# Performance work log

Hardware: AMD Instinct MI355X
Metric: run time of the kernel (lower is better)

The kernel has to match this reference:

```python
import jax, jax.numpy as jnp
import numpy as np

N, E, D_IN, D_OUT = 50000, 800000, 128, 64


def setup_inputs() -> dict:
    key = jax.random.key(0)
    ks = jax.random.split(key, 8)
    s = 1.0 / np.sqrt(D_IN)
    return {
        "x": jax.random.normal(ks[0], (N, D_IN), jnp.float32),
        "edge_index": jax.random.randint(ks[1], (2, E), 0, N),
        "edge_weight": jax.random.uniform(ks[2], (E,), jnp.float32),
        "init_w": jax.random.normal(ks[3], (D_IN, D_IN), jnp.float32) * s,
        "gru_w_ih": jax.random.normal(ks[4], (3 * D_IN, D_IN), jnp.float32) * s,
        "gru_w_hh": jax.random.normal(ks[5], (3 * D_IN, D_IN), jnp.float32) * s,
        "gru_b_ih": jnp.zeros((3 * D_IN,), jnp.float32),
        "gru_b_hh": jnp.zeros((3 * D_IN,), jnp.float32),
        "lin_w": jax.random.normal(ks[6], (D_OUT, D_IN), jnp.float32) * s,
        "lin_b": jnp.zeros((D_OUT,), jnp.float32),
    }


def _gru_step(x, h, w_ih, w_hh, b_ih, b_hh):
    # torch GRU gate order: r, z, n
    gi = x @ w_ih.T + b_ih
    gh = h @ w_hh.T + b_hh
    i_r, i_z, i_n = jnp.split(gi, 3, axis=-1)
    h_r, h_z, h_n = jnp.split(gh, 3, axis=-1)
    r = jax.nn.sigmoid(i_r + h_r)
    z = jax.nn.sigmoid(i_z + h_z)
    n = jnp.tanh(i_n + r * h_n)
    return (1.0 - z) * n + z * h


def reference(x, edge_index, edge_weight, init_w, gru_w_ih, gru_w_hh, gru_b_ih, gru_b_hh, lin_w, lin_b):
    n_nodes = x.shape[0]
    # EvolveGCNO: evolve W via one GRU step, W is both input and hidden (rows = GRU batch)
    W = _gru_step(init_w, init_w, gru_w_ih, gru_w_hh, gru_b_ih, gru_b_hh)  # [D_IN, D_IN]

    # gcn_norm with self-loops (fill value 1.0)
    loop = jnp.arange(n_nodes)
    row = jnp.concatenate([edge_index[0], loop])  # source j
    col = jnp.concatenate([edge_index[1], loop])  # target i
    w = jnp.concatenate([edge_weight, jnp.ones((n_nodes,), x.dtype)])
    deg = jax.ops.segment_sum(w, col, num_segments=n_nodes)
    dis = jnp.where(deg > 0, jax.lax.rsqrt(jnp.maximum(deg, 1e-12)), 0.0)
    norm = dis[row] * w * dis[col]  # [E+N]

    xw = x @ W  # [N, D_IN]
    h = jax.ops.segment_sum(norm[:, None] * xw[row], col, num_segments=n_nodes)
    h = jax.nn.relu(h)
    return h @ lin_w.T + lin_b  # [N, D_OUT]
```

## Files before the change

kernel.cpp:

```cpp
#include <hip/hip_runtime.h>
#include <hip/hip_fp16.h>
#include <math.h>

#define NN 50000
#define NE 800000
#define D  128
#define D3 384
#define DO 64

__global__ __launch_bounds__(256) void gru_matmul_kernel(
    const float* __restrict__ init_w, const float* __restrict__ w_ih,
    const float* __restrict__ w_hh, const float* __restrict__ b_ih,
    const float* __restrict__ b_hh, float* __restrict__ gi, float* __restrict__ gh) {
  int idx = blockIdx.x * 256 + threadIdx.x;
  if (idx >= D * D3) return;
  int b = idx / D3;
  int g = idx % D3;
  const float* xr = init_w + b * D;
  const float* wi = w_ih + g * D;
  const float* wh = w_hh + g * D;
  float ai = 0.f, ah = 0.f;
#pragma unroll 8
  for (int k = 0; k < D; ++k) {
    float xv = xr[k];
    ai += xv * wi[k];
    ah += xv * wh[k];
  }
  gi[idx] = ai + b_ih[g];
  gh[idx] = ah + b_hh[g];
}

__global__ __launch_bounds__(256) void gru_combine_kernel(
    const float* __restrict__ gi, const float* __restrict__ gh,
    const float* __restrict__ init_w, float* __restrict__ W) {
  int idx = blockIdx.x * 256 + threadIdx.x;
  if (idx >= D * D) return;
  int b = idx / D;
  int j = idx % D;
  float ir = gi[b * D3 + j],          hr = gh[b * D3 + j];
  float iz = gi[b * D3 + D + j],      hz = gh[b * D3 + D + j];
  float in_ = gi[b * D3 + 2 * D + j], hn = gh[b * D3 + 2 * D + j];
  float r = 1.f / (1.f + expf(-(ir + hr)));
  float z = 1.f / (1.f + expf(-(iz + hz)));
  float n = tanhf(in_ + r * hn);
  W[idx] = (1.f - z) * n + z * init_w[idx];
}

__global__ __launch_bounds__(256) void init_kernel(unsigned long long* __restrict__ packed,
                                                   int* __restrict__ total) {
  int i = blockIdx.x * 256 + threadIdx.x;
  if (i < NN) packed[i] = (1ULL << 32);
  if (i == 0) *total = 0;
}

__global__ __launch_bounds__(256) void count_deg_kernel(const int* __restrict__ col,
                                                        const float* __restrict__ ew,
                                                        unsigned long long* __restrict__ packed,
                                                        int* __restrict__ rank) {
  int e = blockIdx.x * 256 + threadIdx.x;
  if (e < NE) {
    int c = col[e];
    unsigned long long add =
        (1ULL << 40) | (unsigned long long)(ew[e] * 4294967296.0f);
    unsigned long long old = atomicAdd(&packed[c], add);
    rank[e] = (int)(old >> 40);
  }
}

__global__ __launch_bounds__(256) void dis_scan_kernel(
    const unsigned long long* __restrict__ packed, float* __restrict__ dis,
    int* __restrict__ cnt, int* __restrict__ start, int* __restrict__ total) {
  int i = blockIdx.x * 256 + threadIdx.x;
  int lane = threadIdx.x & 63;
  int c = 0;
  float d = 1.0f;
  if (i < NN) {
    unsigned long long p = packed[i];
    c = (int)(p >> 40);
    d = (float)(p & ((1ULL << 40) - 1)) * 0x1p-32f;
  }
  int pre = c;
#pragma unroll
  for (int off = 1; off < 64; off <<= 1) {
    int t = __shfl_up(pre, off, 64);
    if (lane >= off) pre += t;
  }
  int excl = pre - c;
  int wtot = __shfl(pre, 63, 64);
  int base = 0;
  if (lane == 63) base = atomicAdd(total, wtot);
  base = __shfl(base, 63, 64);
  if (i < NN) {
    start[i] = base + excl;
    cnt[i] = c;
    dis[i] = rsqrtf(fmaxf(d, 1e-12f));
  }
}

__global__ __launch_bounds__(256) void bucket_kernel(
    const int* __restrict__ row, const int* __restrict__ col,
    const float* __restrict__ ew, const int* __restrict__ rank,
    const float* __restrict__ dis, const int* __restrict__ start,
    int2* __restrict__ elist) {
  int e = blockIdx.x * 256 + threadIdx.x;
  if (e >= NE) return;
  int j = row[e];
  int c = col[e];
  float nrm = dis[j] * ew[e] * dis[c];
  int slot = start[c] + rank[e];
  elist[slot] = make_int2(j, __float_as_int(nrm));
}

struct alignas(16) h2x4 { __half2 a, b, c, d; };

__global__ __launch_bounds__(256) void xw_kernel(const float* __restrict__ x,
                                                 const float* __restrict__ W,
                                                 __half* __restrict__ xwh) {
  __shared__ float Wl[D * D];
  for (int i = threadIdx.x; i < D * D; i += 256) Wl[i] = W[i];
  __syncthreads();
  const int t = threadIdx.x;
  const int rr = t >> 4;
  const int c0 = (t & 15) * 8;
  const int ROWS_PER_TILE = 64;
  for (int base = blockIdx.x * ROWS_PER_TILE; base < NN; base += gridDim.x * ROWS_PER_TILE) {
    float acc[4][8];
#pragma unroll
    for (int q = 0; q < 4; ++q)
#pragma unroll
      for (int j = 0; j < 8; ++j) acc[q][j] = 0.f;
    int r0 = base + rr;
#pragma unroll 4
    for (int k = 0; k < D; ++k) {
      float xv[4];
#pragma unroll
      for (int q = 0; q < 4; ++q) {
        int r = r0 + q * 16;
        xv[q] = (r < NN) ? x[(long)r * D + k] : 0.f;
      }
#pragma unroll
      for (int j = 0; j < 8; ++j) {
        float wv = Wl[k * D + c0 + j];
#pragma unroll
        for (int q = 0; q < 4; ++q) acc[q][j] += xv[q] * wv;
      }
    }
#pragma unroll
    for (int q = 0; q < 4; ++q) {
      int r = r0 + q * 16;
      if (r < NN) {
        h2x4 pk;
        pk.a = __floats2half2_rn(acc[q][0], acc[q][1]);
        pk.b = __floats2half2_rn(acc[q][2], acc[q][3]);
        pk.c = __floats2half2_rn(acc[q][4], acc[q][5]);
        pk.d = __floats2half2_rn(acc[q][6], acc[q][7]);
        *(h2x4*)(xwh + (long)r * D + c0) = pk;
      }
    }
  }
}

__global__ __launch_bounds__(256) void gather_out_kernel(
    const int* __restrict__ start, const int* __restrict__ cnt,
    const int2* __restrict__ elist, const float* __restrict__ dis,
    const __half* __restrict__ xwh, const float* __restrict__ lin_w,
    const float* __restrict__ lin_b, float* __restrict__ out) {
  __shared__ __half2 LTh[(D / 2) * DO];
  __shared__ float hb[4][D];
  for (int idx = threadIdx.x; idx < (D / 2) * DO; idx += 256) {
    int kk = idx >> 6, o = idx & 63;
    LTh[idx] = __floats2half2_rn(lin_w[o * D + 2 * kk], lin_w[o * D + 2 * kk + 1]);
  }
  __syncthreads();
  const int wv = threadIdx.x >> 6;
  const int lane = threadIdx.x & 63;
  const float bias = lin_b[lane];
  const __half2* __restrict__ xw2 = (const __half2*)xwh;
  int gw = blockIdx.x * 4 + wv;
  int nw = gridDim.x * 4;
  for (int i = gw; i < NN; i += nw) {
    float ds = dis[i];
    float sn = ds * ds;
    float2 sv = __half22float2(xw2[(long)i * 64 + lane]);
    float a0 = sn * sv.x;
    float a1 = sn * sv.y;
    int s = start[i];
    int se = s + cnt[i];
    for (; s + 4 <= se; s += 4) {
      int2 e0 = elist[s], e1 = elist[s + 1], e2 = elist[s + 2], e3 = elist[s + 3];
      __half2 v0 = xw2[(long)e0.x * 64 + lane];
      __half2 v1 = xw2[(long)e1.x * 64 + lane];
      __half2 v2 = xw2[(long)e2.x * 64 + lane];
      __half2 v3 = xw2[(long)e3.x * 64 + lane];
      float n0 = __int_as_float(e0.y), n1 = __int_as_float(e1.y);
      float n2 = __int_as_float(e2.y), n3 = __int_as_float(e3.y);
      float2 f0 = __half22float2(v0), f1 = __half22float2(v1);
      float2 f2 = __half22float2(v2), f3 = __half22float2(v3);
      a0 += n0 * f0.x + n1 * f1.x + n2 * f2.x + n3 * f3.x;
      a1 += n0 * f0.y + n1 * f1.y + n2 * f2.y + n3 * f3.y;
    }
    for (; s < se; ++s) {
      int2 e0 = elist[s];
      float2 f0 = __half22float2(xw2[(long)e0.x * 64 + lane]);
      float n0 = __int_as_float(e0.y);
      a0 += n0 * f0.x;
      a1 += n0 * f0.y;
    }
    *(float2*)&hb[wv][2 * lane] = make_float2(fmaxf(a0, 0.f), fmaxf(a1, 0.f));
    asm volatile("s_waitcnt lgkmcnt(0)" ::: "memory");
    float acc = bias;
#pragma unroll
    for (int kk = 0; kk < D / 2; ++kk) {
      float2 hv = *(const float2*)&hb[wv][2 * kk];
      float2 wf = __half22float2(LTh[kk * DO + lane]);
      acc += hv.x * wf.x + hv.y * wf.y;
    }
    asm volatile("s_waitcnt lgkmcnt(0)" ::: "memory");
    out[(long)i * DO + lane] = acc;
  }
}

extern "C" void kernel_launch(void* const* d_in, const int* in_sizes, int n_in,
                              void* d_out, int out_size, void* d_ws, size_t ws_size,
                              hipStream_t stream) {
  const float* x      = (const float*)d_in[0];
  const int*   eidx   = (const int*)d_in[1];
  const float* ew     = (const float*)d_in[2];
  const float* init_w = (const float*)d_in[3];
  const float* w_ih   = (const float*)d_in[4];
  const float* w_hh   = (const float*)d_in[5];
  const float* b_ih   = (const float*)d_in[6];
  const float* b_hh   = (const float*)d_in[7];
  const float* lin_w  = (const float*)d_in[8];
  const float* lin_b  = (const float*)d_in[9];
  float* out = (float*)d_out;
  const int* row = eidx;
  const int* col = eidx + NE;

  float* ws    = (float*)d_ws;
  float* W     = ws;
  float* gi    = W + 16384;
  float* gh    = gi + 49152;
  unsigned long long* packed = (unsigned long long*)(gh + 49152);
  float* dis   = (float*)(packed + 50048);
  int*   cnt   = (int*)(dis + 50048);
  int*   strt  = cnt + 50048;
  int*   total = strt + 50048;
  int*   rank  = total + 64;
  int2*  elist = (int2*)(rank + NE);
  __half* xwh  = (__half*)(elist + NE);

  gru_matmul_kernel<<<192, 256, 0, stream>>>(init_w, w_ih, w_hh, b_ih, b_hh, gi, gh);
  gru_combine_kernel<<<64, 256, 0, stream>>>(gi, gh, init_w, W);
  init_kernel<<<(NN + 255) / 256, 256, 0, stream>>>(packed, total);
  count_deg_kernel<<<(NE + 255) / 256, 256, 0, stream>>>(col, ew, packed, rank);
  xw_kernel<<<512, 256, 0, stream>>>(x, W, xwh);
  dis_scan_kernel<<<(NN + 255) / 256, 256, 0, stream>>>(packed, dis, cnt, strt, total);
  bucket_kernel<<<(NE + 255) / 256, 256, 0, stream>>>(row, col, ew, rank, dis, strt,
                                                      elist);
  gather_out_kernel<<<2048, 256, 0, stream>>>(strt, cnt, elist, dis, xwh,
                                              lin_w, lin_b, out);
}
```

Measured before the change: 192.9 us.

## Fuse GRU setup, align edge buckets, split gather from output projection

The two GRU kernels and the init kernel are merged into one setup kernel, so gi/gh no longer round-trip through global memory. Bucket starts are padded to even counts so the gather can read edge pairs with 16-byte vector loads. Streaming loads and stores are marked nontemporal. The gather no longer does the per-node linear layer through LDS: it writes ReLU'd h in fp16, and a separate kernel applies lin_w using fdot2 with the weights held in registers. The cost is an extra fp16 intermediate of N×128 written and read back, plus one more kernel launch.

```diff
diff --git a/kernel.cpp b/kernel.cpp
--- a/kernel.cpp
+++ b/kernel.cpp
@@ -8,49 +8,57 @@
 #define D3 384
 #define DO 64
 
-__global__ __launch_bounds__(256) void gru_matmul_kernel(
+typedef _Float16 f16x2 __attribute__((ext_vector_type(2)));
+
+__device__ __forceinline__ float dot2acc(unsigned int h2bits, f16x2 w, float acc) {
+#if __has_builtin(__builtin_amdgcn_fdot2)
+  return __builtin_amdgcn_fdot2(__builtin_bit_cast(f16x2, h2bits), w, acc, false);
+#else
+  __half2 h = __builtin_bit_cast(__half2, h2bits);
+  float2 hf = __half22float2(h);
+  return acc + hf.x * (float)w[0] + hf.y * (float)w[1];
+#endif
+}
+
+__global__ __launch_bounds__(256) void setup_kernel(
     const float* __restrict__ init_w, const float* __restrict__ w_ih,
     const float* __restrict__ w_hh, const float* __restrict__ b_ih,
-    const float* __restrict__ b_hh, float* __restrict__ gi, float* __restrict__ gh) {
+    const float* __restrict__ b_hh, float* __restrict__ W,
+    unsigned long long* __restrict__ packed, int* __restrict__ total) {
+  if (blockIdx.x >= 64) {
+    int i = (blockIdx.x - 64) * 256 + threadIdx.x;
+    if (i < NN) packed[i] = (1ULL << 32);
+    if (i == 0) *total = 0;
+    return;
+  }
   int idx = blockIdx.x * 256 + threadIdx.x;
-  if (idx >= D * D3) return;
-  int b = idx / D3;
-  int g = idx % D3;
+  int b = idx >> 7;
+  int j = idx & 127;
   const float* xr = init_w + b * D;
-  const float* wi = w_ih + g * D;
-  const float* wh = w_hh + g * D;
-  float ai = 0.f, ah = 0.f;
-#pragma unroll 8
+  const float* wr_i = w_ih + j * D;
+  const float* wz_i = w_ih + (D + j) * D;
+  const float* wn_i = w_ih + (2 * D + j) * D;
+  const float* wr_h = w_hh + j * D;
+  const float* wz_h = w_hh + (D + j) * D;
+  const float* wn_h = w_hh + (2 * D + j) * D;
+  float ir = 0.f, iz = 0.f, in_ = 0.f, hr = 0.f, hz = 0.f, hn = 0.f;
+#pragma unroll 4
   for (int k = 0; k < D; ++k) {
     float xv = xr[k];
-    ai += xv * wi[k];
-    ah += xv * wh[k];
-  }
-  gi[idx] = ai + b_ih[g];
-  gh[idx] = ah + b_hh[g];
-}
-
-__global__ __launch_bounds__(256) void gru_combine_kernel(
-    const float* __restrict__ gi, const float* __restrict__ gh,
-    const float* __restrict__ init_w, float* __restrict__ W) {
-  int idx = blockIdx.x * 256 + threadIdx.x;
-  if (idx >= D * D) return;
-  int b = idx / D;
-  int j = idx % D;
-  float ir = gi[b * D3 + j],          hr = gh[b * D3 + j];
-  float iz = gi[b * D3 + D + j],      hz = gh[b * D3 + D + j];
-  float in_ = gi[b * D3 + 2 * D + j], hn = gh[b * D3 + 2 * D + j];
+    ir += xv * wr_i[k];
+    iz += xv * wz_i[k];
+    in_ += xv * wn_i[k];
+    hr += xv * wr_h[k];
+    hz += xv * wz_h[k];
+    hn += xv * wn_h[k];
+  }
+  ir += b_ih[j];       hr += b_hh[j];
+  iz += b_ih[D + j];   hz += b_hh[D + j];
+  in_ += b_ih[2 * D + j]; hn += b_hh[2 * D + j];
   float r = 1.f / (1.f + expf(-(ir + hr)));
   float z = 1.f / (1.f + expf(-(iz + hz)));
   float n = tanhf(in_ + r * hn);
   W[idx] = (1.f - z) * n + z * init_w[idx];
-}
-
-__global__ __launch_bounds__(256) void init_kernel(unsigned long long* __restrict__ packed,
-                                                   int* __restrict__ total) {
-  int i = blockIdx.x * 256 + threadIdx.x;
-  if (i < NN) packed[i] = (1ULL << 32);
-  if (i == 0) *total = 0;
 }
 
 __global__ __launch_bounds__(256) void count_deg_kernel(const int* __restrict__ col,
@@ -59,11 +67,11 @@
                                                         int* __restrict__ rank) {
   int e = blockIdx.x * 256 + threadIdx.x;
   if (e < NE) {
-    int c = col[e];
-    unsigned long long add =
-        (1ULL << 40) | (unsigned long long)(ew[e] * 4294967296.0f);
+    int c = __builtin_nontemporal_load(&col[e]);
+    float w = __builtin_nontemporal_load(&ew[e]);
+    unsigned long long add = (1ULL << 40) | (unsigned long long)(w * 4294967296.0f);
     unsigned long long old = atomicAdd(&packed[c], add);
-    rank[e] = (int)(old >> 40);
+    __builtin_nontemporal_store((int)(old >> 40), &rank[e]);
   }
 }
 
@@ -79,13 +87,14 @@
     c = (int)(p >> 40);
     d = (float)(p & ((1ULL << 40) - 1)) * 0x1p-32f;
   }
-  int pre = c;
+  int cp = (c + 1) & ~1;
+  int pre = cp;
 #pragma unroll
   for (int off = 1; off < 64; off <<= 1) {
     int t = __shfl_up(pre, off, 64);
     if (lane >= off) pre += t;
   }
-  int excl = pre - c;
+  int excl = pre - cp;
   int wtot = __shfl(pre, 63, 64);
   int base = 0;
   if (lane == 63) base = atomicAdd(total, wtot);
@@ -104,10 +113,12 @@
     int2* __restrict__ elist) {
   int e = blockIdx.x * 256 + threadIdx.x;
   if (e >= NE) return;
-  int j = row[e];
-  int c = col[e];
-  float nrm = dis[j] * ew[e] * dis[c];
-  int slot = start[c] + rank[e];
+  int j = __builtin_nontemporal_load(&row[e]);
+  int c = __builtin_nontemporal_load(&col[e]);
+  float w = __builtin_nontemporal_load(&ew[e]);
+  int rk = __builtin_nontemporal_load(&rank[e]);
+  float nrm = dis[j] * w * dis[c];
+  int slot = start[c] + rk;
   elist[slot] = make_int2(j, __float_as_int(nrm));
 }
 
@@ -160,22 +171,14 @@
   }
 }
 
-__global__ __launch_bounds__(256) void gather_out_kernel(
+__global__ __launch_bounds__(256) void gather_h_kernel(
     const int* __restrict__ start, const int* __restrict__ cnt,
     const int2* __restrict__ elist, const float* __restrict__ dis,
-    const __half* __restrict__ xwh, const float* __restrict__ lin_w,
-    const float* __restrict__ lin_b, float* __restrict__ out) {
-  __shared__ __half2 LTh[(D / 2) * DO];
-  __shared__ float hb[4][D];
-  for (int idx = threadIdx.x; idx < (D / 2) * DO; idx += 256) {
-    int kk = idx >> 6, o = idx & 63;
-    LTh[idx] = __floats2half2_rn(lin_w[o * D + 2 * kk], lin_w[o * D + 2 * kk + 1]);
-  }
-  __syncthreads();
+    const __half* __restrict__ xwh, __half* __restrict__ hout) {
   const int wv = threadIdx.x >> 6;
   const int lane = threadIdx.x & 63;
-  const float bias = lin_b[lane];
   const __half2* __restrict__ xw2 = (const __half2*)xwh;
+  unsigned int* __restrict__ h2u = (unsigned int*)hout;
   int gw = blockIdx.x * 4 + wv;
   int nw = gridDim.x * 4;
   for (int i = gw; i < NN; i += nw) {
@@ -187,13 +190,14 @@
     int s = start[i];
     int se = s + cnt[i];
     for (; s + 4 <= se; s += 4) {
-      int2 e0 = elist[s], e1 = elist[s + 1], e2 = elist[s + 2], e3 = elist[s + 3];
-      __half2 v0 = xw2[(long)e0.x * 64 + lane];
-      __half2 v1 = xw2[(long)e1.x * 64 + lane];
-      __half2 v2 = xw2[(long)e2.x * 64 + lane];
-      __half2 v3 = xw2[(long)e3.x * 64 + lane];
-      float n0 = __int_as_float(e0.y), n1 = __int_as_float(e1.y);
-      float n2 = __int_as_float(e2.y), n3 = __int_as_float(e3.y);
+      uint4 p0 = *(const uint4*)(elist + s);
+      uint4 p1 = *(const uint4*)(elist + s + 2);
+      __half2 v0 = xw2[(long)(int)p0.x * 64 + lane];
+      __half2 v1 = xw2[(long)(int)p0.z * 64 + lane];
+      __half2 v2 = xw2[(long)(int)p1.x * 64 + lane];
+      __half2 v3 = xw2[(long)(int)p1.z * 64 + lane];
+      float n0 = __int_as_float(p0.y), n1 = __int_as_float(p0.w);
+      float n2 = __int_as_float(p1.y), n3 = __int_as_float(p1.w);
       float2 f0 = __half22float2(v0), f1 = __half22float2(v1);
       float2 f2 = __half22float2(v2), f3 = __half22float2(v3);
       a0 += n0 * f0.x + n1 * f1.x + n2 * f2.x + n3 * f3.x;
@@ -206,17 +210,42 @@
       a0 += n0 * f0.x;
       a1 += n0 * f0.y;
     }
-    *(float2*)&hb[wv][2 * lane] = make_float2(fmaxf(a0, 0.f), fmaxf(a1, 0.f));
-    asm volatile("s_waitcnt lgkmcnt(0)" ::: "memory");
+    __half2 hv = __floats2half2_rn(fmaxf(a0, 0.f), fmaxf(a1, 0.f));
+    __builtin_nontemporal_store(__builtin_bit_cast(unsigned int, hv),
+                                &h2u[(long)i * 64 + lane]);
+  }
+}
+
+__global__ __launch_bounds__(256) void out_kernel(
+    const __half* __restrict__ hh, const float* __restrict__ lin_w,
+    const float* __restrict__ lin_b, float* __restrict__ out) {
+  const int wv = threadIdx.x >> 6;
+  const int lane = threadIdx.x & 63;
+  f16x2 lt[64];
+  const float* wrow = lin_w + lane * D;
+#pragma unroll
+  for (int kk = 0; kk < 64; ++kk) {
+    float2 wp = *(const float2*)(wrow + 2 * kk);
+    f16x2 v;
+    v[0] = (_Float16)wp.x;
+    v[1] = (_Float16)wp.y;
+    lt[kk] = v;
+  }
+  const float bias = lin_b[lane];
+  int gw = blockIdx.x * 4 + wv;
+  int nw = gridDim.x * 4;
+  for (int i = gw; i < NN; i += nw) {
+    const uint4* __restrict__ hrow = (const uint4*)(hh + (long)i * D);
     float acc = bias;
 #pragma unroll
-    for (int kk = 0; kk < D / 2; ++kk) {
-      float2 hv = *(const float2*)&hb[wv][2 * kk];
-      float2 wf = __half22float2(LTh[kk * DO + lane]);
-      acc += hv.x * wf.x + hv.y * wf.y;
-    }
-    asm volatile("s_waitcnt lgkmcnt(0)" ::: "memory");
-    out[(long)i * DO + lane] = acc;
+    for (int c = 0; c < 16; ++c) {
+      uint4 v = hrow[c];
+      acc = dot2acc(v.x, lt[4 * c + 0], acc);
+      acc = dot2acc(v.y, lt[4 * c + 1], acc);
+      acc = dot2acc(v.z, lt[4 * c + 2], acc);
+      acc = dot2acc(v.w, lt[4 * c + 3], acc);
+    }
+    __builtin_nontemporal_store(acc, &out[(long)i * DO + lane]);
   }
 }
 
@@ -239,25 +268,23 @@
 
   float* ws    = (float*)d_ws;
   float* W     = ws;
-  float* gi    = W + 16384;
-  float* gh    = gi + 49152;
-  unsigned long long* packed = (unsigned long long*)(gh + 49152);
+  unsigned long long* packed = (unsigned long long*)(W + 16384);
   float* dis   = (float*)(packed + 50048);
   int*   cnt   = (int*)(dis + 50048);
   int*   strt  = cnt + 50048;
   int*   total = strt + 50048;
   int*   rank  = total + 64;
   int2*  elist = (int2*)(rank + NE);
-  __half* xwh  = (__half*)(elist + NE);
-
-  gru_matmul_kernel<<<192, 256, 0, stream>>>(init_w, w_ih, w_hh, b_ih, b_hh, gi, gh);
-  gru_combine_kernel<<<64, 256, 0, stream>>>(gi, gh, init_w, W);
-  init_kernel<<<(NN + 255) / 256, 256, 0, stream>>>(packed, total);
+  __half* xwh  = (__half*)(elist + 850048);
+  __half* hh   = xwh + (long)NN * D;
+
+  setup_kernel<<<64 + (NN + 255) / 256, 256, 0, stream>>>(init_w, w_ih, w_hh, b_ih,
+                                                          b_hh, W, packed, total);
   count_deg_kernel<<<(NE + 255) / 256, 256, 0, stream>>>(col, ew, packed, rank);
   xw_kernel<<<512, 256, 0, stream>>>(x, W, xwh);
   dis_scan_kernel<<<(NN + 255) / 256, 256, 0, stream>>>(packed, dis, cnt, strt, total);
   bucket_kernel<<<(NE + 255) / 256, 256, 0, stream>>>(row, col, ew, rank, dis, strt,
                                                       elist);
-  gather_out_kernel<<<2048, 256, 0, stream>>>(strt, cnt, elist, dis, xwh,
-                                              lin_w, lin_b, out);
-}
+  gather_h_kernel<<<2048, 256, 0, stream>>>(strt, cnt, elist, dis, xwh, hh);
+  out_kernel<<<512, 256, 0, stream>>>(hh, lin_w, lin_b, out);
+}
```

New measurement: 272.4 us. 41.2% more time.
